# Performance work log

Measured on AMD Instinct MI355X. Metric: run time of the kernel, lower is better.

The kernel has to match this reference:

```python
import jax, jax.numpy as jnp
import numpy as np

N, E, B = 50000, 600000, 64


def setup_inputs() -> dict:
    key = jax.random.key(0)
    ks = jax.random.split(key, 24)
    gn = lambda k, shape, s=0.1: jax.random.normal(k, shape, dtype=jnp.float32) * s
    return {
        "x": gn(ks[0], (N, 1), 1.0),
        "edge_index": jax.random.randint(ks[1], (2, E), 0, N),
        "batch": jnp.sort(jax.random.randint(ks[2], (N,), 0, B)),
        # GATConv(1,128)
        "W1": gn(ks[3], (1, 128)), "a1s": gn(ks[4], (128,)), "a1d": gn(ks[5], (128,)), "b1": jnp.zeros((128,), jnp.float32),
        # GATConv(128,128) x2
        "W2": gn(ks[6], (128, 128)), "a2s": gn(ks[7], (128,)), "a2d": gn(ks[8], (128,)), "b2": jnp.zeros((128,), jnp.float32),
        "W3": gn(ks[9], (128, 128)), "a3s": gn(ks[10], (128,)), "a3d": gn(ks[11], (128,)), "b3": jnp.zeros((128,), jnp.float32),
        # GCNConv(128,64), GCNConv(64,32)
        "Wg1": gn(ks[12], (128, 64)), "bg1": jnp.zeros((64,), jnp.float32),
        "Wg2": gn(ks[13], (64, 32)), "bg2": jnp.zeros((32,), jnp.float32),
        # SoftmaxAggregation learnable temperature (init 1.0)
        "t": jnp.ones((), jnp.float32),
        # Linear heads
        "Wl1": gn(ks[14], (32, 16)), "bl1": jnp.zeros((16,), jnp.float32),
        "Wl2": gn(ks[15], (16, 2)), "bl2": jnp.zeros((2,), jnp.float32),
    }


def reference(x, edge_index, batch, W1, a1s, a1d, b1, W2, a2s, a2d, b2,
              W3, a3s, a3d, b3, Wg1, bg1, Wg2, bg2, t, Wl1, bl1, Wl2, bl2):
    # add self-loops (PyG default for GATConv and GCNConv)
    loops = jnp.arange(N)
    ei = jnp.concatenate([edge_index, jnp.stack([loops, loops])], axis=1)
    src, dst = ei[0], ei[1]  # messages flow src -> dst

    def seg_softmax(logits, seg, num):
        m = jax.ops.segment_max(logits, seg, num)
        m = jnp.where(jnp.isfinite(m), m, 0.0)
        e = jnp.exp(logits - m[seg])
        s = jax.ops.segment_sum(e, seg, num)
        return e / (s[seg] + 1e-16)

    def gat(h_in, W, a_src, a_dst, b):
        h = h_in @ W                                   # [N, F]
        logit = jax.nn.leaky_relu((h @ a_src)[src] + (h @ a_dst)[dst], 0.2)
        alpha = seg_softmax(logit, dst, N)             # edge-softmax over neighbors of dst
        return jax.ops.segment_sum(alpha[:, None] * h[src], dst, N) + b

    def gcn(h_in, W, b):
        deg = jax.ops.segment_sum(jnp.ones(src.shape[0], h_in.dtype), dst, N)
        dinv = jnp.where(deg > 0, jax.lax.rsqrt(deg), 0.0)
        norm = dinv[src] * dinv[dst]                   # symmetric normalization
        h = h_in @ W
        return jax.ops.segment_sum(norm[:, None] * h[src], dst, N) + b

    h = jax.nn.elu(gat(x, W1, a1s, a1d, b1))
    h = jax.nn.elu(gat(h, W2, a2s, a2d, b2))
    h = jax.nn.elu(gat(h, W3, a3s, a3d, b3))
    h = jax.nn.elu(gcn(h, Wg1, bg1))
    h = jax.nn.elu(gcn(h, Wg2, bg2))

    # SoftmaxAggregation: per-graph, per-channel softmax weights w = softmax(t*h)
    logits = h * t
    m = jax.ops.segment_max(logits, batch, B)
    m = jnp.where(jnp.isfinite(m), m, 0.0)
    e = jnp.exp(logits - m[batch])
    s = jax.ops.segment_sum(e, batch, B)
    w = e / (s[batch] + 1e-16)
    g = jax.ops.segment_sum(w * h, batch, B)           # [B, 32]

    g = jax.nn.elu(g @ Wl1 + bl1)
    return jax.nn.log_softmax(g @ Wl2 + bl2, axis=1)
```

## Files before the change

### kernel.cpp

```cpp
#include <hip/hip_runtime.h>
#include <math.h>

static inline int cdiv(long a, long b){ return (int)((a + b - 1) / b); }
static inline char* alignp(char* p, size_t a){ return (char*)(((uintptr_t)p + a - 1) & ~(uintptr_t)(a - 1)); }

typedef __attribute__((ext_vector_type(8))) short bf16x8;
typedef __attribute__((ext_vector_type(4))) short bf16x4;
typedef __attribute__((ext_vector_type(4))) float f32x4;

__device__ __forceinline__ float lrelu(float x){ return x > 0.f ? x : 0.2f * x; }
__device__ __forceinline__ float eluf(float x){ return x > 0.f ? x : __expf(x) - 1.f; }
__device__ __forceinline__ short f2bf(float f){
  unsigned u = __float_as_uint(f);
  return (short)((u + 0x7FFFu + ((u >> 16) & 1u)) >> 16);
}
__device__ __forceinline__ float bflo(unsigned v){ return __uint_as_float(v << 16); }
__device__ __forceinline__ float bfhi(unsigned v){ return __uint_as_float(v & 0xFFFF0000u); }

template<int K, int FOUT, bool DOTS>
__global__ void k_gemm_mfma(const short* __restrict__ Abf, const short* __restrict__ Wp,
                            short* __restrict__ outb,
                            const float* __restrict__ av_s, const float* __restrict__ av_d,
                            float* __restrict__ as_, float* __restrict__ ad_, int N){
  constexpr int NKS = K / 32, NCT = FOUT / 16;
  int wid  = threadIdx.x >> 6;
  int lane = threadIdx.x & 63;
  int rowbase = (blockIdx.x * 4 + wid) * 16;
  if(rowbase >= N) return;
  int arow = rowbase + (lane & 15);
  if(arow >= N) arow = N - 1;
  f32x4 acc[NCT] = {};
  const short* ap = Abf + (long)arow * K + (lane >> 4) * 8;
  #pragma unroll
  for(int ks = 0; ks < NKS; ++ks){
    bf16x8 a = *(const bf16x8*)(ap + ks * 32);
    #pragma unroll
    for(int ct = 0; ct < NCT; ++ct){
      bf16x8 b = *(const bf16x8*)(Wp + ((ks * NCT + ct) * 64 + lane) * 8);
      acc[ct] = __builtin_amdgcn_mfma_f32_16x16x32_bf16(a, b, acc[ct], 0, 0, 0);
    }
  }
  int r0 = rowbase + (lane >> 4) * 4;
  int c0 = lane & 15;
  #pragma unroll
  for(int j = 0; j < 4; ++j){
    int r = r0 + j;
    if(r < N){
      #pragma unroll
      for(int ct = 0; ct < NCT; ++ct)
        outb[(long)r * FOUT + ct * 16 + c0] = f2bf(acc[ct][j]);
    }
  }
  if(DOTS){
    float avs[NCT], avd[NCT];
    #pragma unroll
    for(int ct = 0; ct < NCT; ++ct){ avs[ct] = av_s[ct * 16 + c0]; avd[ct] = av_d[ct * 16 + c0]; }
    #pragma unroll
    for(int j = 0; j < 4; ++j){
      float ps = 0.f, pd = 0.f;
      #pragma unroll
      for(int ct = 0; ct < NCT; ++ct){
        float hv = acc[ct][j];
        ps = fmaf(hv, avs[ct], ps);
        pd = fmaf(hv, avd[ct], pd);
      }
      #pragma unroll
      for(int off = 1; off < 16; off <<= 1){
        ps += __shfl_xor(ps, off);
        pd += __shfl_xor(pd, off);
      }
      int r = r0 + j;
      if(c0 == 0 && r < N){ as_[r] = ps; ad_[r] = pd; }
    }
  }
}

template<int K, int FOUT>
__device__ __forceinline__ void pack_dev(const float* __restrict__ W, short* __restrict__ Wp, int idx){
  constexpr int NKS = K / 32, NCT = FOUT / 16;
  if(idx >= NKS * NCT * 64) return;
  int lane = idx & 63;
  int ct = (idx >> 6) % NCT;
  int ks = (idx >> 6) / NCT;
  int col = ct * 16 + (lane & 15);
  int kb  = ks * 32 + (lane >> 4) * 8;
  #pragma unroll
  for(int j = 0; j < 8; ++j) Wp[idx * 8 + j] = f2bf(W[(kb + j) * FOUT + col]);
}
__global__ void k_pack_all(const float* __restrict__ W2, const float* __restrict__ W3,
                           const float* __restrict__ Wg1, const float* __restrict__ Wg2,
                           const float* __restrict__ W1, const float* __restrict__ a1s,
                           const float* __restrict__ a1d,
                           short* __restrict__ Wp2, short* __restrict__ Wp3,
                           short* __restrict__ Wpg1, short* __restrict__ Wpg2,
                           float* __restrict__ S){
  int b = blockIdx.x;
  if(b < 8)       pack_dev<128,128>(W2,  Wp2,  b * 256 + threadIdx.x);
  else if(b < 16) pack_dev<128,128>(W3,  Wp3,  (b - 8) * 256 + threadIdx.x);
  else if(b < 20) pack_dev<128, 64>(Wg1, Wpg1, (b - 16) * 256 + threadIdx.x);
  else if(b == 20) pack_dev<64, 32>(Wg2, Wpg2, threadIdx.x);
  else{
    __shared__ float s1[128], s2[128];
    int t = threadIdx.x;
    if(t < 128){ float w = W1[t]; s1[t] = w * a1s[t]; s2[t] = w * a1d[t]; }
    __syncthreads();
    for(int off = 64; off > 0; off >>= 1){
      if(t < off){ s1[t] += s1[t + off]; s2[t] += s2[t + off]; }
      __syncthreads();
    }
    if(t == 0){ S[0] = s1[0]; S[1] = s2[0]; }
  }
}

__global__ void k_l1v(const float* __restrict__ x, const float* __restrict__ W1,
                      const float* __restrict__ S, short* __restrict__ outb,
                      float* __restrict__ as_, float* __restrict__ ad_, int N){
  long idx = (long)blockIdx.x * blockDim.x + threadIdx.x;
  if(idx >= (long)N * 16) return;
  int node = (int)(idx >> 4), j8 = ((int)idx & 15) * 8;
  float xv = x[node];
  float4 w0 = *(const float4*)(W1 + j8);
  float4 w1 = *(const float4*)(W1 + j8 + 4);
  bf16x8 v;
  v[0] = f2bf(xv * w0.x); v[1] = f2bf(xv * w0.y);
  v[2] = f2bf(xv * w0.z); v[3] = f2bf(xv * w0.w);
  v[4] = f2bf(xv * w1.x); v[5] = f2bf(xv * w1.y);
  v[6] = f2bf(xv * w1.z); v[7] = f2bf(xv * w1.w);
  *(bf16x8*)(outb + (long)node * 128 + j8) = v;
  if((idx & 15) == 0){ as_[node] = xv * S[0]; ad_[node] = xv * S[1]; }
}

__global__ void k_deg_count8(const int* __restrict__ ei, int E, int Pdiv,
                             int* __restrict__ deg){
  int p = blockIdx.x & 7;
  int lo = p * Pdiv, hi = lo + Pdiv;
  long stride = (long)(gridDim.x >> 3) * blockDim.x;
  for(long e = (long)(blockIdx.x >> 3) * blockDim.x + threadIdx.x; e < E; e += stride){
    int d = ei[E + e];
    if(d >= lo && d < hi) atomicAdd(&deg[d], 1);
  }
}

__global__ void k_scan_part(const int* __restrict__ deg, int* __restrict__ bsum, int N){
  __shared__ int red[256];
  int i = blockIdx.x * 256 + threadIdx.x;
  int v = (i < N) ? deg[i] + 1 : 0;
  red[threadIdx.x] = v;
  __syncthreads();
  #pragma unroll
  for(int off = 128; off > 0; off >>= 1){
    if(threadIdx.x < off) red[threadIdx.x] += red[threadIdx.x + off];
    __syncthreads();
  }
  if(threadIdx.x == 0) bsum[blockIdx.x] = red[0];
}
__global__ void k_scan_mid(int* __restrict__ bsum, int NB, int* __restrict__ rowptr, int N){
  __shared__ int buf[1024];
  int t = threadIdx.x;
  int v = (t < NB) ? bsum[t] : 0;
  buf[t] = v;
  __syncthreads();
  for(int off = 1; off < 1024; off <<= 1){
    int u = (t >= off) ? buf[t - off] : 0;
    __syncthreads();
    buf[t] += u;
    __syncthreads();
  }
  if(t < NB) bsum[t] = buf[t] - v;
  if(t == 1023) rowptr[N] = buf[1023];
}
__global__ void k_scan_fin(const int* __restrict__ deg, const int* __restrict__ bsum,
                           int* __restrict__ rowptr, int* __restrict__ cursor,
                           float* __restrict__ dinv, int N){
  __shared__ int buf[256];
  int i = blockIdx.x * 256 + threadIdx.x;
  int t = threadIdx.x;
  int v = (i < N) ? deg[i] + 1 : 0;
  buf[t] = v;
  __syncthreads();
  #pragma unroll
  for(int off = 1; off < 256; off <<= 1){
    int u = (t >= off) ? buf[t - off] : 0;
    __syncthreads();
    buf[t] += u;
    __syncthreads();
  }
  if(i < N){
    int ex = buf[t] - v + bsum[blockIdx.x];
    rowptr[i] = ex; cursor[i] = ex;
    dinv[i] = rsqrtf((float)v);
  }
}

__global__ void k_fill8(const int* __restrict__ ei, int E, int N, int Pdiv,
                        int* __restrict__ cursor, int* __restrict__ csr){
  int p = blockIdx.x & 7;
  int lo = p * Pdiv, hi = lo + Pdiv;
  long ET = (long)E + N;
  long stride = (long)(gridDim.x >> 3) * blockDim.x;
  for(long e = (long)(blockIdx.x >> 3) * blockDim.x + threadIdx.x; e < ET; e += stride){
    int d = (e < E) ? ei[E + e] : (int)(e - E);
    if(d < lo || d >= hi) continue;
    int s = (e < E) ? ei[e] : d;
    int pos = atomicAdd(&cursor[d], 1);
    csr[pos] = s;
  }
}

__global__ void k_gat_agg(const int* __restrict__ rowptr, const int* __restrict__ csr,
                          const float* __restrict__ as_, const float* __restrict__ ad_,
                          const short* __restrict__ h, const float* __restrict__ bias,
                          short* __restrict__ out, int N){
  int pair = (int)(((long)blockIdx.x * blockDim.x + threadIdx.x) >> 6);
  if(pair * 2 >= N) return;
  int lane = threadIdx.x & 63;
  int half = lane >> 5, hl = lane & 31;
  int w = pair * 2 + half;
  bool active = (w < N);
  int start = 0, end = 0, deg = 0;
  float add = 0.f;
  if(active){ start = rowptr[w]; end = rowptr[w + 1]; deg = end - start; add = ad_[w]; }

  int s_reg = 0;
  float logit = -INFINITY;
  if(hl < deg){
    s_reg = csr[start + hl];
    logit = lrelu(as_[s_reg] + add);
  }
  float m, inv, alpha_reg;
  if(deg <= 32){
    m = logit;
    #pragma unroll
    for(int off = 16; off > 0; off >>= 1) m = fmaxf(m, __shfl_xor(m, off));
    float e = __expf(logit - m);
    float ssum = e;
    #pragma unroll
    for(int off = 16; off > 0; off >>= 1) ssum += __shfl_xor(ssum, off);
    inv = 1.f / (ssum + 1e-16f);
    alpha_reg = e * inv;
  }else{
    float mm = logit, ssum = (hl < deg) ? 1.f : 0.f;
    for(int e = start + hl + 32; e < end; e += 32){
      int s = csr[e];
      float l = lrelu(as_[s] + add);
      if(l > mm){ ssum = ssum * __expf(mm - l) + 1.f; mm = l; }
      else        ssum += __expf(l - mm);
    }
    #pragma unroll
    for(int off = 16; off > 0; off >>= 1){
      float mo = __shfl_xor(mm, off);
      float so = __shfl_xor(ssum, off);
      float mn = fmaxf(mm, mo);
      float ea = (mm > -INFINITY) ? __expf(mm - mn) : 0.f;
      float eb = (mo > -INFINITY) ? __expf(mo - mn) : 0.f;
      ssum = ssum * ea + so * eb;
      mm = mn;
    }
    m = mm;
    inv = 1.f / (ssum + 1e-16f);
    alpha_reg = __expf(logit - m) * inv;
  }

  float acc[8] = {};
  int nb = deg < 32 ? deg : 32;
  int gg = hl >> 4;
  int fo = (hl & 15) * 8;
  int base = half << 5;
  const short* hf = h + fo;
  for(int k = 0; k < nb; k += 8){
    uint4 hv[4]; float av[4];
    #pragma unroll
    for(int u = 0; u < 4; ++u){
      int idx = k + 2 * u + gg;
      bool ok = idx < nb;
      int sl = base + (ok ? idx : 0);
      float a = __shfl(alpha_reg, sl);
      av[u] = ok ? a : 0.f;
      int s  = __shfl(s_reg, sl);
      hv[u] = *(const uint4*)(hf + (long)s * 128);
    }
    #pragma unroll
    for(int u = 0; u < 4; ++u){
      acc[0] = fmaf(av[u], bflo(hv[u].x), acc[0]);
      acc[1] = fmaf(av[u], bfhi(hv[u].x), acc[1]);
      acc[2] = fmaf(av[u], bflo(hv[u].y), acc[2]);
      acc[3] = fmaf(av[u], bfhi(hv[u].y), acc[3]);
      acc[4] = fmaf(av[u], bflo(hv[u].z), acc[4]);
      acc[5] = fmaf(av[u], bfhi(hv[u].z), acc[5]);
      acc[6] = fmaf(av[u], bflo(hv[u].w), acc[6]);
      acc[7] = fmaf(av[u], bfhi(hv[u].w), acc[7]);
    }
  }
  for(int e = start + 32; e < end; ++e){
    if(hl < 16){
      int s = csr[e];
      float l = lrelu(as_[s] + add);
      float a = __expf(l - m) * inv;
      uint4 hv = *(const uint4*)(hf + (long)s * 128);
      acc[0] = fmaf(a, bflo(hv.x), acc[0]);
      acc[1] = fmaf(a, bfhi(hv.x), acc[1]);
      acc[2] = fmaf(a, bflo(hv.y), acc[2]);
      acc[3] = fmaf(a, bfhi(hv.y), acc[3]);
      acc[4] = fmaf(a, bflo(hv.z), acc[4]);
      acc[5] = fmaf(a, bfhi(hv.z), acc[5]);
      acc[6] = fmaf(a, bflo(hv.w), acc[6]);
      acc[7] = fmaf(a, bfhi(hv.w), acc[7]);
    }
  }
  #pragma unroll
  for(int j = 0; j < 8; ++j) acc[j] += __shfl_xor(acc[j], 16);
  if(active && hl < 16){
    float4 b0 = *(const float4*)(bias + fo);
    float4 b1 = *(const float4*)(bias + fo + 4);
    bf16x8 v;
    v[0] = f2bf(eluf(acc[0] + b0.x)); v[1] = f2bf(eluf(acc[1] + b0.y));
    v[2] = f2bf(eluf(acc[2] + b0.z)); v[3] = f2bf(eluf(acc[3] + b0.w));
    v[4] = f2bf(eluf(acc[4] + b1.x)); v[5] = f2bf(eluf(acc[5] + b1.y));
    v[6] = f2bf(eluf(acc[6] + b1.z)); v[7] = f2bf(eluf(acc[7] + b1.w));
    *(bf16x8*)(out + (long)w * 128 + fo) = v;
  }
}

template<int F, bool BFOUT>
__global__ void k_gcn_agg(const int* __restrict__ rowptr, const int* __restrict__ csr,
                          const float* __restrict__ dinv, const short* __restrict__ h,
                          const float* __restrict__ bias, short* __restrict__ out_bf,
                          float* __restrict__ out_f, int N){
  constexpr int FPL = F / 16;
  int pair = (int)(((long)blockIdx.x * blockDim.x + threadIdx.x) >> 6);
  if(pair * 2 >= N) return;
  int lane = threadIdx.x & 63;
  int half = lane >> 5, hl = lane & 31;
  int w = pair * 2 + half;
  bool active = (w < N);
  int start = 0, end = 0, deg = 0;
  float dd = 0.f;
  if(active){ start = rowptr[w]; end = rowptr[w + 1]; deg = end - start; dd = dinv[w]; }
  int s_reg = 0; float dv_reg = 0.f;
  if(hl < deg){
    s_reg = csr[start + hl];
    dv_reg = dinv[s_reg];
  }
  float acc[FPL] = {};
  int nb = deg < 32 ? deg : 32;
  int gg = hl >> 4;
  int fo = (hl & 15) * FPL;
  int base = half << 5;
  const short* hf = h + fo;
  for(int k = 0; k < nb; k += 8){
    uint2 hv4[4]; unsigned hv2[4]; float nv[4];
    #pragma unroll
    for(int u = 0; u < 4; ++u){
      int idx = k + 2 * u + gg;
      bool ok = idx < nb;
      int sl = base + (ok ? idx : 0);
      float nrm = dd * __shfl(dv_reg, sl);
      nv[u] = ok ? nrm : 0.f;
      int s = __shfl(s_reg, sl);
      if(FPL == 4) hv4[u] = *(const uint2*)(hf + (long)s * F);
      else         hv2[u] = *(const unsigned*)(hf + (long)s * F);
    }
    #pragma unroll
    for(int u = 0; u < 4; ++u){
      if(FPL == 4){
        acc[0] = fmaf(nv[u], bflo(hv4[u].x), acc[0]);
        acc[1] = fmaf(nv[u], bfhi(hv4[u].x), acc[1]);
        acc[2] = fmaf(nv[u], bflo(hv4[u].y), acc[2]);
        acc[3] = fmaf(nv[u], bfhi(hv4[u].y), acc[3]);
      }else{
        acc[0] = fmaf(nv[u], bflo(hv2[u]), acc[0]);
        acc[1] = fmaf(nv[u], bfhi(hv2[u]), acc[1]);
      }
    }
  }
  for(int e = start + 32; e < end; ++e){
    if(hl < 16){
      int s = csr[e];
      float nrm = dd * dinv[s];
      if(FPL == 4){
        uint2 hv = *(const uint2*)(hf + (long)s * F);
        acc[0] = fmaf(nrm, bflo(hv.x), acc[0]);
        acc[1] = fmaf(nrm, bfhi(hv.x), acc[1]);
        acc[2] = fmaf(nrm, bflo(hv.y), acc[2]);
        acc[3] = fmaf(nrm, bfhi(hv.y), acc[3]);
      }else{
        unsigned hv = *(const unsigned*)(hf + (long)s * F);
        acc[0] = fmaf(nrm, bflo(hv), acc[0]);
        acc[1] = fmaf(nrm, bfhi(hv), acc[1]);
      }
    }
  }
  #pragma unroll
  for(int j = 0; j < FPL; ++j) acc[j] += __shfl_xor(acc[j], 16);
  if(active && hl < 16){
    if(BFOUT){
      if(FPL == 4){
        bf16x4 v;
        #pragma unroll
        for(int j = 0; j < 4; ++j) v[j] = f2bf(eluf(acc[j] + bias[fo + j]));
        *(bf16x4*)(out_bf + (long)w * F + fo) = v;
      }else{
        #pragma unroll
        for(int j = 0; j < FPL; ++j)
          out_bf[(long)w * F + fo + j] = f2bf(eluf(acc[j] + bias[fo + j]));
      }
    }else{
      if(FPL == 2){
        float2 v2 = make_float2(eluf(acc[0] + bias[fo]), eluf(acc[1] + bias[fo + 1]));
        *(float2*)(out_f + (long)w * F + fo) = v2;
      }else{
        #pragma unroll
        for(int j = 0; j < FPL; ++j)
          out_f[(long)w * F + fo + j] = eluf(acc[j] + bias[fo + j]);
      }
    }
  }
}

template<int S>
__global__ void k_bagg_part(const float* __restrict__ h, const int* __restrict__ batch,
                            const float* __restrict__ t, float* __restrict__ pM,
                            float* __restrict__ pS, float* __restrict__ pV, int N){
  int chunk = blockIdx.x;
  int b = chunk / S, s = chunk % S;
  __shared__ int s_lo, s_hi;
  if(threadIdx.x == 0){
    int lo = 0, hi = N;
    while(lo < hi){ int mid = (lo + hi) >> 1; if(batch[mid] < b) lo = mid + 1; else hi = mid; }
    s_lo = lo;
    int lo2 = lo, hi2 = N;
    while(lo2 < hi2){ int mid = (lo2 + hi2) >> 1; if(batch[mid] < b + 1) lo2 = mid + 1; else hi2 = mid; }
    s_hi = lo2;
  }
  __syncthreads();
  int lo = s_lo, hi = s_hi;
  int len = hi - lo;
  int per = (len + S - 1) / S;
  int clo = lo + s * per;
  int chi = clo + per; if(chi > hi) chi = hi;
  float tv = t[0];
  int c = threadIdx.x & 31, r = threadIdx.x >> 5;

  float m = -INFINITY, ss = 0.f, vv = 0.f;
  for(int i = clo + r; i < chi; i += 8){
    float hv = h[(long)i * 32 + c];
    float l = hv * tv;
    if(l > m){
      float e = (m > -INFINITY) ? __expf(m - l) : 0.f;
      ss = ss * e + 1.f; vv = vv * e + hv; m = l;
    }else{
      float e = __expf(l - m);
      ss += e; vv += e * hv;
    }
  }
  __shared__ float rm[8][32], rs[8][32], rv[8][32];
  rm[r][c] = m; rs[r][c] = ss; rv[r][c] = vv;
  __syncthreads();
  if(r == 0){
    float M = rm[0][c], SS = rs[0][c], VV = rv[0][c];
    #pragma unroll
    for(int k = 1; k < 8; ++k){
      float mo = rm[k][c], so = rs[k][c], vo = rv[k][c];
      float mn = fmaxf(M, mo);
      float ea = (M  > -INFINITY) ? __expf(M  - mn) : 0.f;
      float eb = (mo > -INFINITY) ? __expf(mo - mn) : 0.f;
      SS = SS * ea + so * eb; VV = VV * ea + vo * eb; M = mn;
    }
    pM[chunk * 32 + c] = M; pS[chunk * 32 + c] = SS; pV[chunk * 32 + c] = VV;
  }
}
template<int S>
__global__ void k_bagg_comb(const float* __restrict__ pM, const float* __restrict__ pS,
                            const float* __restrict__ pV, float* __restrict__ g, int B){
  int idx = blockIdx.x * blockDim.x + threadIdx.x;
  if(idx >= B * 32) return;
  int b = idx >> 5, c = idx & 31;
  float M = -INFINITY, SS = 0.f, VV = 0.f;
  #pragma unroll 4
  for(int k = 0; k < S; ++k){
    int p = (b * S + k) * 32 + c;
    float mo = pM[p], so = pS[p], vo = pV[p];
    float mn = fmaxf(M, mo);
    float ea = (M  > -INFINITY) ? __expf(M  - mn) : 0.f;
    float eb = (mo > -INFINITY) ? __expf(mo - mn) : 0.f;
    SS = SS * ea + so * eb; VV = VV * ea + vo * eb; M = mn;
  }
  g[idx] = VV / (SS + 1e-16f);
}

__global__ void k_head(const float* __restrict__ g, const float* __restrict__ Wl1,
                       const float* __restrict__ bl1, const float* __restrict__ Wl2,
                       const float* __restrict__ bl2, float* __restrict__ out, int B){
  int b = blockIdx.x * blockDim.x + threadIdx.x;
  if(b >= B) return;
  float gr[32];
  #pragma unroll
  for(int k = 0; k < 32; ++k) gr[k] = g[b * 32 + k];
  float h1[16];
  #pragma unroll
  for(int j = 0; j < 16; ++j){
    float acc = bl1[j];
    #pragma unroll
    for(int k = 0; k < 32; ++k) acc = fmaf(gr[k], Wl1[k * 16 + j], acc);
    h1[j] = eluf(acc);
  }
  float l0 = bl2[0], l1 = bl2[1];
  #pragma unroll
  for(int k = 0; k < 16; ++k){
    l0 = fmaf(h1[k], Wl2[k * 2 + 0], l0);
    l1 = fmaf(h1[k], Wl2[k * 2 + 1], l1);
  }
  float mx = fmaxf(l0, l1);
  float lse = mx + __logf(__expf(l0 - mx) + __expf(l1 - mx));
  out[b * 2 + 0] = l0 - lse;
  out[b * 2 + 1] = l1 - lse;
}

extern "C" void kernel_launch(void* const* d_in, const int* in_sizes, int n_in,
                              void* d_out, int out_size, void* d_ws, size_t ws_size,
                              hipStream_t stream){
  const float* x     = (const float*)d_in[0];
  const int*   ei    = (const int*)d_in[1];
  const int*   batch = (const int*)d_in[2];
  const float* W1 = (const float*)d_in[3];
  const float* a1s = (const float*)d_in[4];
  const float* a1d = (const float*)d_in[5];
  const float* b1 = (const float*)d_in[6];
  const float* W2 = (const float*)d_in[7];
  const float* a2s = (const float*)d_in[8];
  const float* a2d = (const float*)d_in[9];
  const float* b2 = (const float*)d_in[10];
  const float* W3 = (const float*)d_in[11];
  const float* a3s = (const float*)d_in[12];
  const float* a3d = (const float*)d_in[13];
  const float* b3 = (const float*)d_in[14];
  const float* Wg1 = (const float*)d_in[15];
  const float* bg1 = (const float*)d_in[16];
  const float* Wg2 = (const float*)d_in[17];
  const float* bg2 = (const float*)d_in[18];
  const float* t   = (const float*)d_in[19];
  const float* Wl1 = (const float*)d_in[20];
  const float* bl1 = (const float*)d_in[21];
  const float* Wl2 = (const float*)d_in[22];
  const float* bl2 = (const float*)d_in[23];

  const int N = in_sizes[0];
  const int E = in_sizes[1] / 2;
  const int B = out_size / 2;
  const int ET = E + N;
  float* out = (float*)d_out;
  constexpr int BS = 32;

  char* p = (char*)d_ws;
  short* Hbf  = (short*)p;            p += (size_t)N * 128 * 2;
  short* Abf  = (short*)p;            p += (size_t)N * 128 * 2;
  float* A32  = (float*)p;            p += (size_t)N * 32 * 4;
  float* as_  = (float*)p;            p += (size_t)N * 4;
  float* ad_  = (float*)p;            p += (size_t)N * 4;
  float* dinv = (float*)p;            p += (size_t)N * 4;
  int*   deg    = (int*)p;            p += (size_t)N * 4;
  int*   rowptr = (int*)p;            p += (size_t)(N + 1) * 4;
  int*   cursor = (int*)p;            p += (size_t)N * 4;
  int*   csr    = (int*)p;            p += (size_t)ET * 4;
  int*   bsum   = (int*)p;            p += (size_t)1024 * 4;
  p = alignp(p, 16);
  short* Wp2  = (short*)p;            p += 128 * 128 * 2;
  short* Wp3  = (short*)p;            p += 128 * 128 * 2;
  short* Wpg1 = (short*)p;            p += 128 * 64 * 2;
  short* Wpg2 = (short*)p;            p += 64 * 32 * 2;
  p = alignp(p, 16);
  float* S    = (float*)p;            p += 16 * 4;
  float* pM   = (float*)p;            p += (size_t)B * BS * 32 * 4;
  float* pSb  = (float*)p;            p += (size_t)B * BS * 32 * 4;
  float* pV   = (float*)p;            p += (size_t)B * BS * 32 * 4;
  float* g    = (float*)p;

  const int T = 256;
  const int gW2  = cdiv((long)N * 32, T);
  const int gG   = cdiv(N, 64);
  const int NB   = cdiv(N, 256);
  const int Pdiv = cdiv(N, 8);

  hipMemsetAsync(deg, 0, (size_t)N * 4, stream);
  k_deg_count8<<<dim3(2048), dim3(T), 0, stream>>>(ei, E, Pdiv, deg);
  k_scan_part<<<dim3(NB), dim3(256), 0, stream>>>(deg, bsum, N);
  k_scan_mid<<<dim3(1), dim3(1024), 0, stream>>>(bsum, NB, rowptr, N);
  k_scan_fin<<<dim3(NB), dim3(256), 0, stream>>>(deg, bsum, rowptr, cursor, dinv, N);
  k_fill8<<<dim3(2048), dim3(T), 0, stream>>>(ei, E, N, Pdiv, cursor, csr);
  k_pack_all<<<dim3(22), dim3(T), 0, stream>>>(W2, W3, Wg1, Wg2, W1, a1s, a1d,
                                               Wp2, Wp3, Wpg1, Wpg2, S);

  k_l1v<<<dim3(cdiv((long)N * 16, T)), dim3(T), 0, stream>>>(x, W1, S, Hbf, as_, ad_, N);
  k_gat_agg<<<dim3(gW2), dim3(T), 0, stream>>>(rowptr, csr, as_, ad_, Hbf, b1, Abf, N);

  k_gemm_mfma<128,128,true><<<dim3(gG), dim3(T), 0, stream>>>(Abf, Wp2, Hbf, a2s, a2d, as_, ad_, N);
  k_gat_agg<<<dim3(gW2), dim3(T), 0, stream>>>(rowptr, csr, as_, ad_, Hbf, b2, Abf, N);

  k_gemm_mfma<128,128,true><<<dim3(gG), dim3(T), 0, stream>>>(Abf, Wp3, Hbf, a3s, a3d, as_, ad_, N);
  k_gat_agg<<<dim3(gW2), dim3(T), 0, stream>>>(rowptr, csr, as_, ad_, Hbf, b3, Abf, N);

  k_gemm_mfma<128,64,false><<<dim3(gG), dim3(T), 0, stream>>>(Abf, Wpg1, Hbf, nullptr, nullptr, nullptr, nullptr, N);
  k_gcn_agg<64,true><<<dim3(gW2), dim3(T), 0, stream>>>(rowptr, csr, dinv, Hbf, bg1, Abf, (float*)nullptr, N);

  k_gemm_mfma<64,32,false><<<dim3(gG), dim3(T), 0, stream>>>(Abf, Wpg2, Hbf, nullptr, nullptr, nullptr, nullptr, N);
  k_gcn_agg<32,false><<<dim3(gW2), dim3(T), 0, stream>>>(rowptr, csr, dinv, Hbf, bg2, (short*)nullptr, A32, N);

  k_bagg_part<BS><<<dim3(B * BS), dim3(256), 0, stream>>>(A32, batch, t, pM, pSb, pV, N);
  k_bagg_comb<BS><<<dim3(cdiv(B * 32, 256)), dim3(256), 0, stream>>>(pM, pSb, pV, g, B);

  k_head<<<dim3(cdiv(B, 64)), dim3(64), 0, stream>>>(g, Wl1, bl1, Wl2, bl2, out, B);
}
```

Measured before the change: 258.1 us.

## Fuse prep/layer1 and final kernels, double GEMM row tiles, deepen gather unroll

Several ideas land together. The weight packing and layer-1 projection are merged into one launch, with each block recomputing the attention scalars locally. The batch-combine and head kernels are merged into a single 1024-thread block. Each GEMM wave now handles 32 rows so every loaded weight fragment feeds two MFMAs, and the GAT/GCN gather loops issue 8 neighbor loads per iteration instead of 4. The aim is fewer launches and more memory-level parallelism, at the cost of more registers and redundant shared reductions in every prep block.

```diff
diff --git a/kernel.cpp b/kernel.cpp
--- a/kernel.cpp
+++ b/kernel.cpp
@@ -25,30 +25,41 @@
   constexpr int NKS = K / 32, NCT = FOUT / 16;
   int wid  = threadIdx.x >> 6;
   int lane = threadIdx.x & 63;
-  int rowbase = (blockIdx.x * 4 + wid) * 16;
+  int rowbase = (blockIdx.x * 4 + wid) * 32;
   if(rowbase >= N) return;
-  int arow = rowbase + (lane & 15);
-  if(arow >= N) arow = N - 1;
-  f32x4 acc[NCT] = {};
-  const short* ap = Abf + (long)arow * K + (lane >> 4) * 8;
+  int arow0 = rowbase + (lane & 15);
+  int arow1 = rowbase + 16 + (lane & 15);
+  if(arow0 >= N) arow0 = N - 1;
+  if(arow1 >= N) arow1 = N - 1;
+  f32x4 acc0[NCT] = {}, acc1[NCT] = {};
+  const short* ap0 = Abf + (long)arow0 * K + (lane >> 4) * 8;
+  const short* ap1 = Abf + (long)arow1 * K + (lane >> 4) * 8;
   #pragma unroll
   for(int ks = 0; ks < NKS; ++ks){
-    bf16x8 a = *(const bf16x8*)(ap + ks * 32);
+    bf16x8 a0 = *(const bf16x8*)(ap0 + ks * 32);
+    bf16x8 a1 = *(const bf16x8*)(ap1 + ks * 32);
     #pragma unroll
     for(int ct = 0; ct < NCT; ++ct){
       bf16x8 b = *(const bf16x8*)(Wp + ((ks * NCT + ct) * 64 + lane) * 8);
-      acc[ct] = __builtin_amdgcn_mfma_f32_16x16x32_bf16(a, b, acc[ct], 0, 0, 0);
-    }
-  }
-  int r0 = rowbase + (lane >> 4) * 4;
+      acc0[ct] = __builtin_amdgcn_mfma_f32_16x16x32_bf16(a0, b, acc0[ct], 0, 0, 0);
+      acc1[ct] = __builtin_amdgcn_mfma_f32_16x16x32_bf16(a1, b, acc1[ct], 0, 0, 0);
+    }
+  }
+  int rq = (lane >> 4) * 4;
   int c0 = lane & 15;
   #pragma unroll
   for(int j = 0; j < 4; ++j){
-    int r = r0 + j;
+    int r = rowbase + rq + j;
     if(r < N){
       #pragma unroll
       for(int ct = 0; ct < NCT; ++ct)
-        outb[(long)r * FOUT + ct * 16 + c0] = f2bf(acc[ct][j]);
+        outb[(long)r * FOUT + ct * 16 + c0] = f2bf(acc0[ct][j]);
+    }
+    int r1 = rowbase + 16 + rq + j;
+    if(r1 < N){
+      #pragma unroll
+      for(int ct = 0; ct < NCT; ++ct)
+        outb[(long)r1 * FOUT + ct * 16 + c0] = f2bf(acc1[ct][j]);
     }
   }
   if(DOTS){
@@ -60,7 +71,7 @@
       float ps = 0.f, pd = 0.f;
       #pragma unroll
       for(int ct = 0; ct < NCT; ++ct){
-        float hv = acc[ct][j];
+        float hv = acc0[ct][j];
         ps = fmaf(hv, avs[ct], ps);
         pd = fmaf(hv, avd[ct], pd);
       }
@@ -69,7 +80,24 @@
         ps += __shfl_xor(ps, off);
         pd += __shfl_xor(pd, off);
       }
-      int r = r0 + j;
+      int r = rowbase + rq + j;
+      if(c0 == 0 && r < N){ as_[r] = ps; ad_[r] = pd; }
+    }
+    #pragma unroll
+    for(int j = 0; j < 4; ++j){
+      float ps = 0.f, pd = 0.f;
+      #pragma unroll
+      for(int ct = 0; ct < NCT; ++ct){
+        float hv = acc1[ct][j];
+        ps = fmaf(hv, avs[ct], ps);
+        pd = fmaf(hv, avd[ct], pd);
+      }
+      #pragma unroll
+      for(int off = 1; off < 16; off <<= 1){
+        ps += __shfl_xor(ps, off);
+        pd += __shfl_xor(pd, off);
+      }
+      int r = rowbase + 16 + rq + j;
       if(c0 == 0 && r < N){ as_[r] = ps; ad_[r] = pd; }
     }
   }
@@ -87,35 +115,29 @@
   #pragma unroll
   for(int j = 0; j < 8; ++j) Wp[idx * 8 + j] = f2bf(W[(kb + j) * FOUT + col]);
 }
-__global__ void k_pack_all(const float* __restrict__ W2, const float* __restrict__ W3,
-                           const float* __restrict__ Wg1, const float* __restrict__ Wg2,
-                           const float* __restrict__ W1, const float* __restrict__ a1s,
-                           const float* __restrict__ a1d,
-                           short* __restrict__ Wp2, short* __restrict__ Wp3,
-                           short* __restrict__ Wpg1, short* __restrict__ Wpg2,
-                           float* __restrict__ S){
+__global__ void k_prep(const float* __restrict__ W2, const float* __restrict__ W3,
+                       const float* __restrict__ Wg1, const float* __restrict__ Wg2,
+                       const float* __restrict__ W1, const float* __restrict__ a1s,
+                       const float* __restrict__ a1d, const float* __restrict__ x,
+                       short* __restrict__ Wp2, short* __restrict__ Wp3,
+                       short* __restrict__ Wpg1, short* __restrict__ Wpg2,
+                       short* __restrict__ outb, float* __restrict__ as_,
+                       float* __restrict__ ad_, int N){
   int b = blockIdx.x;
-  if(b < 8)       pack_dev<128,128>(W2,  Wp2,  b * 256 + threadIdx.x);
-  else if(b < 16) pack_dev<128,128>(W3,  Wp3,  (b - 8) * 256 + threadIdx.x);
-  else if(b < 20) pack_dev<128, 64>(Wg1, Wpg1, (b - 16) * 256 + threadIdx.x);
-  else if(b == 20) pack_dev<64, 32>(Wg2, Wpg2, threadIdx.x);
-  else{
-    __shared__ float s1[128], s2[128];
-    int t = threadIdx.x;
-    if(t < 128){ float w = W1[t]; s1[t] = w * a1s[t]; s2[t] = w * a1d[t]; }
+  if(b < 8){       pack_dev<128,128>(W2,  Wp2,  b * 256 + threadIdx.x); return; }
+  if(b < 16){      pack_dev<128,128>(W3,  Wp3,  (b - 8) * 256 + threadIdx.x); return; }
+  if(b < 20){      pack_dev<128, 64>(Wg1, Wpg1, (b - 16) * 256 + threadIdx.x); return; }
+  if(b == 20){     pack_dev< 64, 32>(Wg2, Wpg2, threadIdx.x); return; }
+  __shared__ float s1[128], s2[128];
+  int t = threadIdx.x;
+  if(t < 128){ float w = W1[t]; s1[t] = w * a1s[t]; s2[t] = w * a1d[t]; }
+  __syncthreads();
+  for(int off = 64; off > 0; off >>= 1){
+    if(t < off){ s1[t] += s1[t + off]; s2[t] += s2[t + off]; }
     __syncthreads();
-    for(int off = 64; off > 0; off >>= 1){
-      if(t < off){ s1[t] += s1[t + off]; s2[t] += s2[t + off]; }
-      __syncthreads();
-    }
-    if(t == 0){ S[0] = s1[0]; S[1] = s2[0]; }
-  }
-}
-
-__global__ void k_l1v(const float* __restrict__ x, const float* __restrict__ W1,
-                      const float* __restrict__ S, short* __restrict__ outb,
-                      float* __restrict__ as_, float* __restrict__ ad_, int N){
-  long idx = (long)blockIdx.x * blockDim.x + threadIdx.x;
+  }
+  float S0 = s1[0], S1 = s2[0];
+  long idx = (long)(b - 21) * blockDim.x + t;
   if(idx >= (long)N * 16) return;
   int node = (int)(idx >> 4), j8 = ((int)idx & 15) * 8;
   float xv = x[node];
@@ -127,7 +149,7 @@
   v[4] = f2bf(xv * w1.x); v[5] = f2bf(xv * w1.y);
   v[6] = f2bf(xv * w1.z); v[7] = f2bf(xv * w1.w);
   *(bf16x8*)(outb + (long)node * 128 + j8) = v;
-  if((idx & 15) == 0){ as_[node] = xv * S[0]; ad_[node] = xv * S[1]; }
+  if((idx & 15) == 0){ as_[node] = xv * S0; ad_[node] = xv * S1; }
 }
 
 __global__ void k_deg_count8(const int* __restrict__ ei, int E, int Pdiv,
@@ -267,10 +289,10 @@
   int fo = (hl & 15) * 8;
   int base = half << 5;
   const short* hf = h + fo;
-  for(int k = 0; k < nb; k += 8){
-    uint4 hv[4]; float av[4];
-    #pragma unroll
-    for(int u = 0; u < 4; ++u){
+  for(int k = 0; k < nb; k += 16){
+    uint4 hv[8]; float av[8];
+    #pragma unroll
+    for(int u = 0; u < 8; ++u){
       int idx = k + 2 * u + gg;
       bool ok = idx < nb;
       int sl = base + (ok ? idx : 0);
@@ -280,7 +302,7 @@
       hv[u] = *(const uint4*)(hf + (long)s * 128);
     }
     #pragma unroll
-    for(int u = 0; u < 4; ++u){
+    for(int u = 0; u < 8; ++u){
       acc[0] = fmaf(av[u], bflo(hv[u].x), acc[0]);
       acc[1] = fmaf(av[u], bfhi(hv[u].x), acc[1]);
       acc[2] = fmaf(av[u], bflo(hv[u].y), acc[2]);
@@ -347,10 +369,10 @@
   int fo = (hl & 15) * FPL;
   int base = half << 5;
   const short* hf = h + fo;
-  for(int k = 0; k < nb; k += 8){
-    uint2 hv4[4]; unsigned hv2[4]; float nv[4];
-    #pragma unroll
-    for(int u = 0; u < 4; ++u){
+  for(int k = 0; k < nb; k += 16){
+    uint2 hv4[8]; unsigned hv2[8]; float nv[8];
+    #pragma unroll
+    for(int u = 0; u < 8; ++u){
       int idx = k + 2 * u + gg;
       bool ok = idx < nb;
       int sl = base + (ok ? idx : 0);
@@ -361,7 +383,7 @@
       else         hv2[u] = *(const unsigned*)(hf + (long)s * F);
     }
     #pragma unroll
-    for(int u = 0; u < 4; ++u){
+    for(int u = 0; u < 8; ++u){
       if(FPL == 4){
         acc[0] = fmaf(nv[u], bflo(hv4[u].x), acc[0]);
         acc[1] = fmaf(nv[u], bfhi(hv4[u].x), acc[1]);
@@ -469,51 +491,52 @@
     pM[chunk * 32 + c] = M; pS[chunk * 32 + c] = SS; pV[chunk * 32 + c] = VV;
   }
 }
+
 template<int S>
-__global__ void k_bagg_comb(const float* __restrict__ pM, const float* __restrict__ pS,
-                            const float* __restrict__ pV, float* __restrict__ g, int B){
-  int idx = blockIdx.x * blockDim.x + threadIdx.x;
-  if(idx >= B * 32) return;
-  int b = idx >> 5, c = idx & 31;
-  float M = -INFINITY, SS = 0.f, VV = 0.f;
-  #pragma unroll 4
-  for(int k = 0; k < S; ++k){
-    int p = (b * S + k) * 32 + c;
-    float mo = pM[p], so = pS[p], vo = pV[p];
-    float mn = fmaxf(M, mo);
-    float ea = (M  > -INFINITY) ? __expf(M  - mn) : 0.f;
-    float eb = (mo > -INFINITY) ? __expf(mo - mn) : 0.f;
-    SS = SS * ea + so * eb; VV = VV * ea + vo * eb; M = mn;
-  }
-  g[idx] = VV / (SS + 1e-16f);
-}
-
-__global__ void k_head(const float* __restrict__ g, const float* __restrict__ Wl1,
-                       const float* __restrict__ bl1, const float* __restrict__ Wl2,
-                       const float* __restrict__ bl2, float* __restrict__ out, int B){
-  int b = blockIdx.x * blockDim.x + threadIdx.x;
-  if(b >= B) return;
-  float gr[32];
-  #pragma unroll
-  for(int k = 0; k < 32; ++k) gr[k] = g[b * 32 + k];
-  float h1[16];
-  #pragma unroll
-  for(int j = 0; j < 16; ++j){
-    float acc = bl1[j];
-    #pragma unroll
-    for(int k = 0; k < 32; ++k) acc = fmaf(gr[k], Wl1[k * 16 + j], acc);
-    h1[j] = eluf(acc);
-  }
-  float l0 = bl2[0], l1 = bl2[1];
-  #pragma unroll
-  for(int k = 0; k < 16; ++k){
-    l0 = fmaf(h1[k], Wl2[k * 2 + 0], l0);
-    l1 = fmaf(h1[k], Wl2[k * 2 + 1], l1);
-  }
-  float mx = fmaxf(l0, l1);
-  float lse = mx + __logf(__expf(l0 - mx) + __expf(l1 - mx));
-  out[b * 2 + 0] = l0 - lse;
-  out[b * 2 + 1] = l1 - lse;
+__global__ void k_final(const float* __restrict__ pM, const float* __restrict__ pS,
+                        const float* __restrict__ pV, const float* __restrict__ Wl1,
+                        const float* __restrict__ bl1, const float* __restrict__ Wl2,
+                        const float* __restrict__ bl2, float* __restrict__ out, int B){
+  __shared__ float gs[4096];
+  int t = threadIdx.x;
+  for(int idx = t; idx < B * 32; idx += 1024){
+    int b = idx >> 5, c = idx & 31;
+    float M = -INFINITY, SS = 0.f, VV = 0.f;
+    #pragma unroll 4
+    for(int k = 0; k < S; ++k){
+      int p = (b * S + k) * 32 + c;
+      float mo = pM[p], so = pS[p], vo = pV[p];
+      float mn = fmaxf(M, mo);
+      float ea = (M  > -INFINITY) ? __expf(M  - mn) : 0.f;
+      float eb = (mo > -INFINITY) ? __expf(mo - mn) : 0.f;
+      SS = SS * ea + so * eb; VV = VV * ea + vo * eb; M = mn;
+    }
+    gs[idx] = VV / (SS + 1e-16f);
+  }
+  __syncthreads();
+  if(t < B){
+    float gr[32];
+    #pragma unroll
+    for(int k = 0; k < 32; ++k) gr[k] = gs[t * 32 + k];
+    float h1[16];
+    #pragma unroll
+    for(int j = 0; j < 16; ++j){
+      float acc = bl1[j];
+      #pragma unroll
+      for(int k = 0; k < 32; ++k) acc = fmaf(gr[k], Wl1[k * 16 + j], acc);
+      h1[j] = eluf(acc);
+    }
+    float l0 = bl2[0], l1 = bl2[1];
+    #pragma unroll
+    for(int k = 0; k < 16; ++k){
+      l0 = fmaf(h1[k], Wl2[k * 2 + 0], l0);
+      l1 = fmaf(h1[k], Wl2[k * 2 + 1], l1);
+    }
+    float mx = fmaxf(l0, l1);
+    float lse = mx + __logf(__expf(l0 - mx) + __expf(l1 - mx));
+    out[t * 2 + 0] = l0 - lse;
+    out[t * 2 + 1] = l1 - lse;
+  }
 }
 
 extern "C" void kernel_launch(void* const* d_in, const int* in_sizes, int n_in,
@@ -569,15 +592,13 @@
   short* Wpg1 = (short*)p;            p += 128 * 64 * 2;
   short* Wpg2 = (short*)p;            p += 64 * 32 * 2;
   p = alignp(p, 16);
-  float* S    = (float*)p;            p += 16 * 4;
   float* pM   = (float*)p;            p += (size_t)B * BS * 32 * 4;
   float* pSb  = (float*)p;            p += (size_t)B * BS * 32 * 4;
   float* pV   = (float*)p;            p += (size_t)B * BS * 32 * 4;
-  float* g    = (float*)p;
 
   const int T = 256;
   const int gW2  = cdiv((long)N * 32, T);
-  const int gG   = cdiv(N, 64);
+  const int gG   = cdiv(N, 128);
   const int NB   = cdiv(N, 256);
   const int Pdiv = cdiv(N, 8);
 
@@ -587,10 +608,9 @@
   k_scan_mid<<<dim3(1), dim3(1024), 0, stream>>>(bsum, NB, rowptr, N);
   k_scan_fin<<<dim3(NB), dim3(256), 0, stream>>>(deg, bsum, rowptr, cursor, dinv, N);
   k_fill8<<<dim3(2048), dim3(T), 0, stream>>>(ei, E, N, Pdiv, cursor, csr);
-  k_pack_all<<<dim3(22), dim3(T), 0, stream>>>(W2, W3, Wg1, Wg2, W1, a1s, a1d,
-                                               Wp2, Wp3, Wpg1, Wpg2, S);
-
-  k_l1v<<<dim3(cdiv((long)N * 16, T)), dim3(T), 0, stream>>>(x, W1, S, Hbf, as_, ad_, N);
+
+  k_prep<<<dim3(21 + cdiv((long)N * 16, T)), dim3(T), 0, stream>>>(
+      W2, W3, Wg1, Wg2, W1, a1s, a1d, x, Wp2, Wp3, Wpg1, Wpg2, Hbf, as_, ad_, N);
   k_gat_agg<<<dim3(gW2), dim3(T), 0, stream>>>(rowptr, csr, as_, ad_, Hbf, b1, Abf, N);
 
   k_gemm_mfma<128,128,true><<<dim3(gG), dim3(T), 0, stream>>>(Abf, Wp2, Hbf, a2s, a2d, as_, ad_, N);
@@ -606,7 +626,5 @@
   k_gcn_agg<32,false><<<dim3(gW2), dim3(T), 0, stream>>>(rowptr, csr, dinv, Hbf, bg2, (short*)nullptr, A32, N);
 
   k_bagg_part<BS><<<dim3(B * BS), dim3(256), 0, stream>>>(A32, batch, t, pM, pSb, pV, N);
-  k_bagg_comb<BS><<<dim3(cdiv(B * 32, 256)), dim3(256), 0, stream>>>(pM, pSb, pV, g, B);
-
-  k_head<<<dim3(cdiv(B, 64)), dim3(64), 0, stream>>>(g, Wl1, bl1, Wl2, bl2, out, B);
-}
+  k_final<BS><<<dim3(1), dim3(1024), 0, stream>>>(pM, pSb, pV, Wl1, bl1, Wl2, bl2, out, B);
+}
```

Result: slower. 277.4 us (+7.5%).
